# Kernel tuning notes

Measured on AMD Instinct MI355X. Metric: run time of the kernel, lower is better.

The kernel has to match this reference:

```python
import jax, jax.numpy as jnp
import numpy as np

N = 10000      # nodes
E = 160000     # edges (before self-loops)
IN = 128       # input channels
H1, C1 = 8, 128   # layer-1 heads / per-head channels
OUT = 64       # output channels
NEG_SLOPE = 0.2   # PyG GATConv leaky_relu slope


def _glorot(key, shape):
    fan = shape[0] + shape[-1]
    return jax.random.normal(key, shape, jnp.float32) * np.float32(np.sqrt(2.0 / fan))


def setup_inputs() -> dict:
    key = jax.random.key(0)
    ks = jax.random.split(key, 10)
    x = jax.random.normal(ks[0], (N, IN), jnp.float32)
    edge_index = jax.random.randint(ks[1], (2, E), 0, N, dtype=jnp.int64)
    return {
        "x": x,
        "edge_index": edge_index,
        "W1": _glorot(ks[2], (IN, H1 * C1)),
        "a_src1": _glorot(ks[3], (H1, C1)),
        "a_dst1": _glorot(ks[4], (H1, C1)),
        "b1": jnp.zeros((H1 * C1,), jnp.float32),
        "W2": _glorot(ks[5], (H1 * C1, OUT)),
        "a_src2": _glorot(ks[6], (1, OUT)),
        "a_dst2": _glorot(ks[7], (1, OUT)),
        "b2": jnp.zeros((OUT,), jnp.float32),
    }


def gat_conv(x, src, dst, W, a_src, a_dst, bias, heads, ch, concat):
    n = x.shape[0]
    h = (x @ W).reshape(n, heads, ch)                 # [N,H,C]
    alpha_s = jnp.sum(h * a_src, axis=-1)             # [N,H]
    alpha_d = jnp.sum(h * a_dst, axis=-1)             # [N,H]
    e = jax.nn.leaky_relu(alpha_s[src] + alpha_d[dst], NEG_SLOPE)  # [E',H]
    # segment softmax over incoming edges of each dst node
    m = jax.ops.segment_max(e, dst, num_segments=n)
    e = jnp.exp(e - m[dst])
    s = jax.ops.segment_sum(e, dst, num_segments=n)
    alpha = e / (s[dst] + 1e-16)                      # [E',H]
    msg = h[src] * alpha[:, :, None]                  # [E',H,C]
    out = jax.ops.segment_sum(msg, dst, num_segments=n)  # [N,H,C]
    out = out.reshape(n, heads * ch) if concat else jnp.mean(out, axis=1)
    return out + bias


def reference(x, edge_index, W1, a_src1, a_dst1, b1, W2, a_src2, a_dst2, b2):
    n = x.shape[0]
    loops = jnp.arange(n, dtype=edge_index.dtype)     # PyG add_self_loops=True
    src = jnp.concatenate([edge_index[0], loops])
    dst = jnp.concatenate([edge_index[1], loops])
    h = jax.nn.elu(gat_conv(x, src, dst, W1, a_src1, a_dst1, b1, H1, C1, True))
    # dropout is identity in eval mode
    return gat_conv(h, src, dst, W2, a_src2, a_dst2, b2, 1, OUT, False)
```

## Files before the change

### kernel.cpp

```cpp
#include <hip/hip_runtime.h>
#include <math.h>


#define NEG_SLOPE 0.2f

typedef short bf16x8 __attribute__((ext_vector_type(8)));
typedef float f32x4 __attribute__((ext_vector_type(4)));

__device__ __forceinline__ float leaky(float v) { return v >= 0.0f ? v : NEG_SLOPE * v; }

__device__ __forceinline__ unsigned short f2bf(float f) {
    unsigned u = __float_as_uint(f);
    u += 0x7FFFu + ((u >> 16) & 1u);
    return (unsigned short)(u >> 16);
}


__global__ __launch_bounds__(256) void prep_count(
    const float* __restrict__ W1, const float* __restrict__ a_src1,
    const float* __restrict__ a_dst1, const float* __restrict__ W2,
    const int* __restrict__ ei,
    float* __restrict__ As_t, float* __restrict__ Ad_t,
    unsigned short* __restrict__ W1bT, unsigned short* __restrict__ W2bT,
    int* __restrict__ counts, int E, int N) {
    int b = blockIdx.x;
    __shared__ unsigned short tile[32][33];
    if (b < 4) {
        int i = b * 256 + threadIdx.x;
        int k = i >> 3, h = i & 7;
        float ss = 0.f, sd = 0.f;
        for (int c = 0; c < 128; c += 4) {
            float4 w = *(const float4*)(W1 + (size_t)k * 1024 + h * 128 + c);
            float4 a = *(const float4*)(a_src1 + h * 128 + c);
            float4 d = *(const float4*)(a_dst1 + h * 128 + c);
            ss += w.x * a.x + w.y * a.y + w.z * a.z + w.w * a.w;
            sd += w.x * d.x + w.y * d.y + w.z * d.z + w.w * d.w;
        }
        As_t[h * 132 + k] = ss;
        Ad_t[h * 132 + k] = sd;
    } else if (b < 132) {
        int bb = b - 4;
        int kt = bb & 3, hct = bb >> 2;
        int j = threadIdx.x & 31;
        int i0 = threadIdx.x >> 5;
        for (int i = i0; i < 32; i += 8)
            tile[i][j] = f2bf(W1[(size_t)(kt * 32 + i) * 1024 + hct * 32 + j]);
        __syncthreads();
        for (int i = i0; i < 32; i += 8) {
            int hc = hct * 32 + i, k = kt * 32 + j;
            int h = hc >> 7, c = hc & 127;
            W1bT[h * 16384 + c * 128 + k] = tile[j][i];
        }
    } else if (b < 196) {
        int bb = b - 132;
        int kt = bb & 31, ctile = bb >> 5;
        int j = threadIdx.x & 31;
        int i0 = threadIdx.x >> 5;
        for (int i = i0; i < 32; i += 8)
            tile[i][j] = f2bf(W2[(size_t)(kt * 32 + i) * 64 + ctile * 32 + j]);
        __syncthreads();
        for (int i = i0; i < 32; i += 8)
            W2bT[(size_t)(ctile * 32 + i) * 1024 + kt * 32 + j] = tile[j][i];
    } else {
        int i = (b - 196) * 256 + threadIdx.x;
        int M = E + N;
        if (i >= M) return;
        int dst = (i < E) ? ei[E + i] : (i - E);
        atomicAdd(&counts[dst], 1);
    }
}


__global__ __launch_bounds__(1024) void alpha_scan(
    const float* __restrict__ x, const float* __restrict__ As_t, const float* __restrict__ Ad_t,
    float* __restrict__ as1, float* __restrict__ ad1,
    const int* __restrict__ counts, int* __restrict__ offsets,
    int* __restrict__ cursor, int N, int nb_alpha) {
    int t = threadIdx.x;
    if ((int)blockIdx.x < nb_alpha) {
        __shared__ float sAs[1056], sAd[1056];
        for (int i = t; i < 1056; i += 1024) {
            sAs[i] = As_t[i];
            sAd[i] = Ad_t[i];
        }
        __syncthreads();
        int node = blockIdx.x * 128 + (t >> 3);
        int h = t & 7;
        if (node >= N) return;
        const float* sa = sAs + h * 132;
        const float* sd = sAd + h * 132;
        float accs = 0.f, accd = 0.f;
        for (int k = 0; k < 128; k += 4) {
            float4 xv = *(const float4*)(x + (size_t)node * 128 + k);
            float4 av = *(const float4*)(sa + k);
            float4 dv = *(const float4*)(sd + k);
            accs += xv.x * av.x + xv.y * av.y + xv.z * av.z + xv.w * av.w;
            accd += xv.x * dv.x + xv.y * dv.y + xv.z * dv.z + xv.w * dv.w;
        }
        as1[node * 8 + h] = accs;
        ad1[node * 8 + h] = accd;
    } else {
        __shared__ int wsum[16];
        int per = (N + 1023) / 1024;
        int base = t * per;
        int s = 0;
        for (int j = 0; j < per; j++) {
            int idx = base + j;
            if (idx < N) s += counts[idx];
        }
        int lane = t & 63, wid = t >> 6;
        int inc = s;
#pragma unroll
        for (int off = 1; off <= 32; off <<= 1) {
            int v = __shfl_up(inc, off);
            if (lane >= off) inc += v;
        }
        if (lane == 63) wsum[wid] = inc;
        __syncthreads();
        if (t < 16) {
            int v = wsum[t];
            int iv = v;
#pragma unroll
            for (int off = 1; off <= 8; off <<= 1) {
                int u = __shfl_up(iv, off);
                if (t >= off) iv += u;
            }
            wsum[t] = iv - v;
        }
        __syncthreads();
        int run = wsum[wid] + inc - s;
        for (int j = 0; j < per; j++) {
            int idx = base + j;
            if (idx < N) {
                offsets[idx] = run;
                cursor[idx] = run;
                run += counts[idx];
            }
        }
        if (t == 1023) offsets[N] = run;
    }
}


__global__ __launch_bounds__(256) void fill_w1(
    const int* __restrict__ ei, int* __restrict__ cursor,
    const float* __restrict__ as1, const float* __restrict__ ad1,
    int* __restrict__ srcs, float* __restrict__ wbuf, int E, int N) {
    int i = blockIdx.x * blockDim.x + threadIdx.x;
    int M = E + N;
    if (i >= M) return;
    int src, dst;
    if (i < E) { src = ei[i]; dst = ei[E + i]; }
    else       { src = dst = i - E; }
    int pos = atomicAdd(&cursor[dst], 1);
    srcs[pos] = src;
    float4 a0 = *(const float4*)(as1 + (size_t)src * 8);
    float4 a1 = *(const float4*)(as1 + (size_t)src * 8 + 4);
    float4 b0 = *(const float4*)(ad1 + (size_t)dst * 8);
    float4 b1 = *(const float4*)(ad1 + (size_t)dst * 8 + 4);
    float4 w0, w1;
    w0.x = __expf(leaky(a0.x + b0.x));
    w0.y = __expf(leaky(a0.y + b0.y));
    w0.z = __expf(leaky(a0.z + b0.z));
    w0.w = __expf(leaky(a0.w + b0.w));
    w1.x = __expf(leaky(a1.x + b1.x));
    w1.y = __expf(leaky(a1.y + b1.y));
    w1.z = __expf(leaky(a1.z + b1.z));
    w1.w = __expf(leaky(a1.w + b1.w));
    *(float4*)(wbuf + (size_t)pos * 8)     = w0;
    *(float4*)(wbuf + (size_t)pos * 8 + 4) = w1;
}


__global__ __launch_bounds__(256) void l1_gather(
    const float* __restrict__ x, const float* __restrict__ wbuf,
    const int* __restrict__ offsets, const int* __restrict__ srcs,
    unsigned short* __restrict__ y_b, int N) {
    int n = blockIdx.x * 4 + (threadIdx.x >> 6);
    if (n >= N) return;
    int lane = threadIdx.x & 63;
    int beg = offsets[n];
    int deg = offsets[n + 1] - beg;
    float2 acc[8];
#pragma unroll
    for (int h = 0; h < 8; h++) acc[h] = make_float2(0.f, 0.f);
    float4 ws0 = make_float4(0.f, 0.f, 0.f, 0.f);
    float4 ws1 = make_float4(0.f, 0.f, 0.f, 0.f);
    const float* xb = x + lane * 2;
#define L1G_BODY(I)                                                              \
    {                                                                            \
        int s_ = srcs[beg + (I)];                                                \
        float4 w0_ = *(const float4*)(wbuf + (size_t)(beg + (I)) * 8);           \
        float4 w1_ = *(const float4*)(wbuf + (size_t)(beg + (I)) * 8 + 4);       \
        float2 xv_ = *(const float2*)(xb + (size_t)s_ * 128);                    \
        ws0.x += w0_.x; ws0.y += w0_.y; ws0.z += w0_.z; ws0.w += w0_.w;          \
        ws1.x += w1_.x; ws1.y += w1_.y; ws1.z += w1_.z; ws1.w += w1_.w;          \
        acc[0].x = fmaf(w0_.x, xv_.x, acc[0].x); acc[0].y = fmaf(w0_.x, xv_.y, acc[0].y); \
        acc[1].x = fmaf(w0_.y, xv_.x, acc[1].x); acc[1].y = fmaf(w0_.y, xv_.y, acc[1].y); \
        acc[2].x = fmaf(w0_.z, xv_.x, acc[2].x); acc[2].y = fmaf(w0_.z, xv_.y, acc[2].y); \
        acc[3].x = fmaf(w0_.w, xv_.x, acc[3].x); acc[3].y = fmaf(w0_.w, xv_.y, acc[3].y); \
        acc[4].x = fmaf(w1_.x, xv_.x, acc[4].x); acc[4].y = fmaf(w1_.x, xv_.y, acc[4].y); \
        acc[5].x = fmaf(w1_.y, xv_.x, acc[5].x); acc[5].y = fmaf(w1_.y, xv_.y, acc[5].y); \
        acc[6].x = fmaf(w1_.z, xv_.x, acc[6].x); acc[6].y = fmaf(w1_.z, xv_.y, acc[6].y); \
        acc[7].x = fmaf(w1_.w, xv_.x, acc[7].x); acc[7].y = fmaf(w1_.w, xv_.y, acc[7].y); \
    }
    int i = 0;
    for (; i + 4 <= deg; i += 4) {
        L1G_BODY(i) L1G_BODY(i + 1) L1G_BODY(i + 2) L1G_BODY(i + 3)
    }
    for (; i < deg; i++) { L1G_BODY(i) }
#undef L1G_BODY
    float inv[8] = {1.f / (ws0.x + 1e-16f), 1.f / (ws0.y + 1e-16f),
                    1.f / (ws0.z + 1e-16f), 1.f / (ws0.w + 1e-16f),
                    1.f / (ws1.x + 1e-16f), 1.f / (ws1.y + 1e-16f),
                    1.f / (ws1.z + 1e-16f), 1.f / (ws1.w + 1e-16f)};
    unsigned short* dst = y_b + (size_t)n * 1024 + lane * 2;
#pragma unroll
    for (int h = 0; h < 8; h++) {
        unsigned lo = f2bf(acc[h].x * inv[h]);
        unsigned hi = f2bf(acc[h].y * inv[h]);
        *(unsigned*)(dst + h * 128) = lo | (hi << 16);
    }
}


__global__ __launch_bounds__(256) void l12_gemm(
    const unsigned short* __restrict__ y_b, const unsigned short* __restrict__ W1bT,
    const float* __restrict__ b1, const unsigned short* __restrict__ W2bT,
    const float* __restrict__ a_src2, const float* __restrict__ a_dst2,
    float* __restrict__ h2, float* __restrict__ as2, float* __restrict__ ad2, int N) {
    int nb = blockIdx.x * 16;
    int w = threadIdx.x >> 6;
    int lane = threadIdx.x & 63;
    int n16 = lane & 15, quad = lane >> 4;
    __shared__ unsigned short hb[16 * 1032];
    __shared__ float sA[4][16], sD[4][16];
    int node_a = nb + n16;
    const unsigned short* yrow = y_b + (size_t)(node_a < N ? node_a : 0) * 1024;
#pragma unroll
    for (int cti = 0; cti < 16; cti++) {
        int ct = w * 16 + cti;
        int h = ct >> 3;
        int cc = (ct & 7) * 16;
        const unsigned short* Wh = W1bT + h * 16384 + (size_t)(cc + n16) * 128 + quad * 8;
        const unsigned short* ya = yrow + h * 128 + quad * 8;
        f32x4 acc = (f32x4){0.f, 0.f, 0.f, 0.f};
#pragma unroll
        for (int ks = 0; ks < 4; ks++) {
            bf16x8 a = *(const bf16x8*)(ya + ks * 32);
            bf16x8 b = *(const bf16x8*)(Wh + ks * 32);
            acc = __builtin_amdgcn_mfma_f32_16x16x32_bf16(a, b, acc, 0, 0, 0);
        }
        int c = h * 128 + cc + n16;
        float bias = b1[c];
#pragma unroll
        for (int r = 0; r < 4; r++) {
            float v = acc[r] + bias;
            v = v > 0.f ? v : expm1f(v);
            hb[(quad * 4 + r) * 1032 + c] = f2bf(v);
        }
    }
    __syncthreads();
    const unsigned short* arow = hb + n16 * 1032 + quad * 8;
    const unsigned short* brow = W2bT + (size_t)(w * 16 + n16) * 1024 + quad * 8;
    f32x4 acc = (f32x4){0.f, 0.f, 0.f, 0.f};
#pragma unroll 8
    for (int ks = 0; ks < 32; ks++) {
        bf16x8 a = *(const bf16x8*)(arow + ks * 32);
        bf16x8 b = *(const bf16x8*)(brow + ks * 32);
        acc = __builtin_amdgcn_mfma_f32_16x16x32_bf16(a, b, acc, 0, 0, 0);
    }
    int c2 = w * 16 + n16;
    float asc = a_src2[c2], adc = a_dst2[c2];
    float pav[4], pdv[4];
#pragma unroll
    for (int r = 0; r < 4; r++) {
        int node = nb + quad * 4 + r;
        if (node < N) h2[(size_t)node * 64 + c2] = acc[r];
        pav[r] = acc[r] * asc;
        pdv[r] = acc[r] * adc;
#pragma unroll
        for (int mm = 1; mm <= 8; mm <<= 1) {
            pav[r] += __shfl_xor(pav[r], mm);
            pdv[r] += __shfl_xor(pdv[r], mm);
        }
    }
    if (n16 == 0) {
#pragma unroll
        for (int r = 0; r < 4; r++) {
            sA[w][quad * 4 + r] = pav[r];
            sD[w][quad * 4 + r] = pdv[r];
        }
    }
    __syncthreads();
    if (threadIdx.x < 16) {
        int node = nb + threadIdx.x;
        if (node < N) {
            as2[node] = sA[0][threadIdx.x] + sA[1][threadIdx.x] + sA[2][threadIdx.x] + sA[3][threadIdx.x];
            ad2[node] = sD[0][threadIdx.x] + sD[1][threadIdx.x] + sD[2][threadIdx.x] + sD[3][threadIdx.x];
        }
    }
}


__global__ __launch_bounds__(256) void l2_gather(
    const float* __restrict__ h2, const float* __restrict__ as2,
    const float* __restrict__ ad2, const float* __restrict__ b2,
    const int* __restrict__ offsets, const int* __restrict__ srcs,
    float* __restrict__ out, int N) {
    int n = blockIdx.x * 4 + (threadIdx.x >> 6);
    if (n >= N) return;
    int lane = threadIdx.x & 63;
    int beg = offsets[n];
    int deg = offsets[n + 1] - beg;
    float adn = ad2[n];
    float acc = 0.f, wsum = 0.f;
    int i = 0;
    for (; i + 4 <= deg; i += 4) {
        int s0 = srcs[beg + i],     s1 = srcs[beg + i + 1];
        int s2 = srcs[beg + i + 2], s3 = srcs[beg + i + 3];
        float w0 = __expf(leaky(as2[s0] + adn));
        float w1 = __expf(leaky(as2[s1] + adn));
        float w2 = __expf(leaky(as2[s2] + adn));
        float w3 = __expf(leaky(as2[s3] + adn));
        float v0 = h2[(size_t)s0 * 64 + lane];
        float v1 = h2[(size_t)s1 * 64 + lane];
        float v2 = h2[(size_t)s2 * 64 + lane];
        float v3 = h2[(size_t)s3 * 64 + lane];
        wsum += w0 + w1 + w2 + w3;
        acc = fmaf(w0, v0, acc);
        acc = fmaf(w1, v1, acc);
        acc = fmaf(w2, v2, acc);
        acc = fmaf(w3, v3, acc);
    }
    for (; i < deg; i++) {
        int s = srcs[beg + i];
        float w = __expf(leaky(as2[s] + adn));
        wsum += w;
        acc = fmaf(w, h2[(size_t)s * 64 + lane], acc);
    }
    out[(size_t)n * 64 + lane] = acc / (wsum + 1e-16f) + b2[lane];
}


static inline size_t align_up(size_t v, size_t a) { return (v + a - 1) / a * a; }

extern "C" void kernel_launch(void* const* d_in, const int* in_sizes, int n_in,
                              void* d_out, int out_size, void* d_ws, size_t ws_size,
                              hipStream_t stream) {
    const float* x      = (const float*)d_in[0];
    const int*   ei     = (const int*)d_in[1];
    const float* W1     = (const float*)d_in[2];
    const float* a_src1 = (const float*)d_in[3];
    const float* a_dst1 = (const float*)d_in[4];
    const float* b1     = (const float*)d_in[5];
    const float* W2     = (const float*)d_in[6];
    const float* a_src2 = (const float*)d_in[7];
    const float* a_dst2 = (const float*)d_in[8];
    const float* b2     = (const float*)d_in[9];
    float* out = (float*)d_out;

    int N = in_sizes[0] / 128;
    int E = in_sizes[1] / 2;
    int M = E + N;

    char* p = (char*)d_ws;
    size_t off = 0;
    auto carve = [&](size_t bytes) {
        void* r = p + off;
        off = align_up(off + bytes, 256);
        return r;
    };
    int*            counts  = (int*)carve((size_t)N * 4);
    int*            offsets = (int*)carve((size_t)(N + 1) * 4);
    int*            cursor  = (int*)carve((size_t)N * 4);
    int*            srcs    = (int*)carve((size_t)M * 4);
    float*          As_t    = (float*)carve(1056 * 4);
    float*          Ad_t    = (float*)carve(1056 * 4);
    float*          as1     = (float*)carve((size_t)N * 8 * 4);
    float*          ad1     = (float*)carve((size_t)N * 8 * 4);
    float*          as2     = (float*)carve((size_t)N * 4);
    float*          ad2     = (float*)carve((size_t)N * 4);
    float*          h2      = (float*)carve((size_t)N * 64 * 4);
    float*          wbuf    = (float*)carve((size_t)M * 8 * 4);
    unsigned short* W1bT    = (unsigned short*)carve((size_t)8 * 128 * 128 * 2);
    unsigned short* W2bT    = (unsigned short*)carve((size_t)64 * 1024 * 2);
    unsigned short* y_b     = (unsigned short*)carve((size_t)N * 1024 * 2);
    (void)ws_size;

    int nb_count = (M + 255) / 256;
    int nb_alpha = (N + 127) / 128;

    hipMemsetAsync(counts, 0, (size_t)N * 4, stream);
    prep_count<<<196 + nb_count, 256, 0, stream>>>(W1, a_src1, a_dst1, W2, ei,
                                                   As_t, Ad_t, W1bT, W2bT, counts, E, N);
    alpha_scan<<<nb_alpha + 1, 1024, 0, stream>>>(x, As_t, Ad_t, as1, ad1,
                                                  counts, offsets, cursor, N, nb_alpha);
    fill_w1<<<nb_count, 256, 0, stream>>>(ei, cursor, as1, ad1, srcs, wbuf, E, N);
    l1_gather<<<(N + 3) / 4, 256, 0, stream>>>(x, wbuf, offsets, srcs, y_b, N);
    l12_gemm<<<(N + 15) / 16, 256, 0, stream>>>(y_b, W1bT, b1, W2bT, a_src2, a_dst2,
                                                h2, as2, ad2, N);
    l2_gather<<<(N + 3) / 4, 256, 0, stream>>>(h2, as2, ad2, b2, offsets, srcs, out, N);
}
```

Before: 192.7 us.

## Fuse layer-1 gather into GEMM kernel via LDS and shuffle-broadcast edge sources

Merges the layer-1 neighbor aggregation into the layer-1/2 GEMM kernel. Each block aggregates its 16 nodes into shared memory instead of writing bf16 rows to a global buffer, which removes one launch and the global write and read of y_b. In both gathers, each lane loads one edge source index and the index is broadcast with wave shuffles instead of repeated scalar loads. The layer-2 gather also computes one attention weight per lane and reduces the sum with xor shuffles. The cost is that the fused kernel roughly doubles its LDS use (about 66KB per block), which can lower occupancy. Each wave also processes its four nodes one after another, so gather latency is less hidden.

Measured after the change: 204.5 us. 6.1% more time.

```diff
diff --git a/kernel.cpp b/kernel.cpp
--- a/kernel.cpp
+++ b/kernel.cpp
@@ -172,27 +172,36 @@
 }
 
 
-__global__ __launch_bounds__(256) void l1_gather(
+__global__ __launch_bounds__(256) void l1g12(
     const float* __restrict__ x, const float* __restrict__ wbuf,
     const int* __restrict__ offsets, const int* __restrict__ srcs,
-    unsigned short* __restrict__ y_b, int N) {
-    int n = blockIdx.x * 4 + (threadIdx.x >> 6);
-    if (n >= N) return;
+    const unsigned short* __restrict__ W1bT, const float* __restrict__ b1,
+    const unsigned short* __restrict__ W2bT,
+    const float* __restrict__ a_src2, const float* __restrict__ a_dst2,
+    float* __restrict__ h2, float* __restrict__ as2, float* __restrict__ ad2, int N) {
+    int nb = blockIdx.x * 16;
+    int w = threadIdx.x >> 6;
     int lane = threadIdx.x & 63;
-    int beg = offsets[n];
-    int deg = offsets[n + 1] - beg;
-    float2 acc[8];
-#pragma unroll
-    for (int h = 0; h < 8; h++) acc[h] = make_float2(0.f, 0.f);
-    float4 ws0 = make_float4(0.f, 0.f, 0.f, 0.f);
-    float4 ws1 = make_float4(0.f, 0.f, 0.f, 0.f);
+    int n16 = lane & 15, quad = lane >> 4;
+    __shared__ unsigned short yls[16 * 1032];
+    __shared__ unsigned short hb[16 * 1032];
+    __shared__ float sA[4][16], sD[4][16];
+
     const float* xb = x + lane * 2;
-#define L1G_BODY(I)                                                              \
+    for (int j = 0; j < 4; j++) {
+        int n = nb + w * 4 + j;
+        float2 acc[8];
+#pragma unroll
+        for (int h = 0; h < 8; h++) acc[h] = make_float2(0.f, 0.f);
+        float4 ws0 = make_float4(0.f, 0.f, 0.f, 0.f);
+        float4 ws1 = make_float4(0.f, 0.f, 0.f, 0.f);
+        int beg = 0, deg = 0;
+        if (n < N) { beg = offsets[n]; deg = offsets[n + 1] - beg; }
+#define L1_FMA(EIDX, SRC)                                                        \
     {                                                                            \
-        int s_ = srcs[beg + (I)];                                                \
-        float4 w0_ = *(const float4*)(wbuf + (size_t)(beg + (I)) * 8);           \
-        float4 w1_ = *(const float4*)(wbuf + (size_t)(beg + (I)) * 8 + 4);       \
-        float2 xv_ = *(const float2*)(xb + (size_t)s_ * 128);                    \
+        float4 w0_ = *(const float4*)(wbuf + (size_t)(EIDX) * 8);                \
+        float4 w1_ = *(const float4*)(wbuf + (size_t)(EIDX) * 8 + 4);            \
+        float2 xv_ = *(const float2*)(xb + (size_t)(SRC) * 128);                 \
         ws0.x += w0_.x; ws0.y += w0_.y; ws0.z += w0_.z; ws0.w += w0_.w;          \
         ws1.x += w1_.x; ws1.y += w1_.y; ws1.z += w1_.z; ws1.w += w1_.w;          \
         acc[0].x = fmaf(w0_.x, xv_.x, acc[0].x); acc[0].y = fmaf(w0_.x, xv_.y, acc[0].y); \
@@ -204,39 +213,45 @@
         acc[6].x = fmaf(w1_.z, xv_.x, acc[6].x); acc[6].y = fmaf(w1_.z, xv_.y, acc[6].y); \
         acc[7].x = fmaf(w1_.w, xv_.x, acc[7].x); acc[7].y = fmaf(w1_.w, xv_.y, acc[7].y); \
     }
-    int i = 0;
-    for (; i + 4 <= deg; i += 4) {
-        L1G_BODY(i) L1G_BODY(i + 1) L1G_BODY(i + 2) L1G_BODY(i + 3)
-    }
-    for (; i < deg; i++) { L1G_BODY(i) }
-#undef L1G_BODY
-    float inv[8] = {1.f / (ws0.x + 1e-16f), 1.f / (ws0.y + 1e-16f),
-                    1.f / (ws0.z + 1e-16f), 1.f / (ws0.w + 1e-16f),
-                    1.f / (ws1.x + 1e-16f), 1.f / (ws1.y + 1e-16f),
-                    1.f / (ws1.z + 1e-16f), 1.f / (ws1.w + 1e-16f)};
-    unsigned short* dst = y_b + (size_t)n * 1024 + lane * 2;
-#pragma unroll
-    for (int h = 0; h < 8; h++) {
-        unsigned lo = f2bf(acc[h].x * inv[h]);
-        unsigned hi = f2bf(acc[h].y * inv[h]);
-        *(unsigned*)(dst + h * 128) = lo | (hi << 16);
-    }
-}
-
-
-__global__ __launch_bounds__(256) void l12_gemm(
-    const unsigned short* __restrict__ y_b, const unsigned short* __restrict__ W1bT,
-    const float* __restrict__ b1, const unsigned short* __restrict__ W2bT,
-    const float* __restrict__ a_src2, const float* __restrict__ a_dst2,
-    float* __restrict__ h2, float* __restrict__ as2, float* __restrict__ ad2, int N) {
-    int nb = blockIdx.x * 16;
-    int w = threadIdx.x >> 6;
-    int lane = threadIdx.x & 63;
-    int n16 = lane & 15, quad = lane >> 4;
-    __shared__ unsigned short hb[16 * 1032];
-    __shared__ float sA[4][16], sD[4][16];
-    int node_a = nb + n16;
-    const unsigned short* yrow = y_b + (size_t)(node_a < N ? node_a : 0) * 1024;
+        if (deg <= 64) {
+            int sv = srcs[beg + (lane < deg ? lane : 0)];
+            int i = 0;
+            for (; i + 4 <= deg; i += 4) {
+                int s0 = __shfl(sv, i);
+                int s1 = __shfl(sv, i + 1);
+                int s2 = __shfl(sv, i + 2);
+                int s3 = __shfl(sv, i + 3);
+                L1_FMA(beg + i, s0)
+                L1_FMA(beg + i + 1, s1)
+                L1_FMA(beg + i + 2, s2)
+                L1_FMA(beg + i + 3, s3)
+            }
+            for (; i < deg; i++) {
+                int s = __shfl(sv, i);
+                L1_FMA(beg + i, s)
+            }
+        } else {
+            for (int i = 0; i < deg; i++) {
+                int s = srcs[beg + i];
+                L1_FMA(beg + i, s)
+            }
+        }
+#undef L1_FMA
+        float inv[8] = {1.f / (ws0.x + 1e-16f), 1.f / (ws0.y + 1e-16f),
+                        1.f / (ws0.z + 1e-16f), 1.f / (ws0.w + 1e-16f),
+                        1.f / (ws1.x + 1e-16f), 1.f / (ws1.y + 1e-16f),
+                        1.f / (ws1.z + 1e-16f), 1.f / (ws1.w + 1e-16f)};
+        unsigned short* drow = &yls[(w * 4 + j) * 1032 + lane * 2];
+#pragma unroll
+        for (int h = 0; h < 8; h++) {
+            unsigned lo = f2bf(acc[h].x * inv[h]);
+            unsigned hi = f2bf(acc[h].y * inv[h]);
+            *(unsigned*)(drow + h * 128) = lo | (hi << 16);
+        }
+    }
+    __syncthreads();
+
+    const unsigned short* yrow = &yls[n16 * 1032];
 #pragma unroll
     for (int cti = 0; cti < 16; cti++) {
         int ct = w * 16 + cti;
@@ -261,6 +276,7 @@
         }
     }
     __syncthreads();
+
     const unsigned short* arow = hb + n16 * 1032 + quad * 8;
     const unsigned short* brow = W2bT + (size_t)(w * 16 + n16) * 1024 + quad * 8;
     f32x4 acc = (f32x4){0.f, 0.f, 0.f, 0.f};
@@ -314,30 +330,42 @@
     int beg = offsets[n];
     int deg = offsets[n + 1] - beg;
     float adn = ad2[n];
-    float acc = 0.f, wsum = 0.f;
-    int i = 0;
-    for (; i + 4 <= deg; i += 4) {
-        int s0 = srcs[beg + i],     s1 = srcs[beg + i + 1];
-        int s2 = srcs[beg + i + 2], s3 = srcs[beg + i + 3];
-        float w0 = __expf(leaky(as2[s0] + adn));
-        float w1 = __expf(leaky(as2[s1] + adn));
-        float w2 = __expf(leaky(as2[s2] + adn));
-        float w3 = __expf(leaky(as2[s3] + adn));
-        float v0 = h2[(size_t)s0 * 64 + lane];
-        float v1 = h2[(size_t)s1 * 64 + lane];
-        float v2 = h2[(size_t)s2 * 64 + lane];
-        float v3 = h2[(size_t)s3 * 64 + lane];
-        wsum += w0 + w1 + w2 + w3;
-        acc = fmaf(w0, v0, acc);
-        acc = fmaf(w1, v1, acc);
-        acc = fmaf(w2, v2, acc);
-        acc = fmaf(w3, v3, acc);
-    }
-    for (; i < deg; i++) {
-        int s = srcs[beg + i];
-        float w = __expf(leaky(as2[s] + adn));
-        wsum += w;
-        acc = fmaf(w, h2[(size_t)s * 64 + lane], acc);
+    float acc = 0.f, wsum;
+    if (deg <= 64) {
+        int sv = srcs[beg + (lane < deg ? lane : 0)];
+        float wv = (lane < deg) ? __expf(leaky(as2[sv] + adn)) : 0.f;
+        int i = 0;
+        for (; i + 4 <= deg; i += 4) {
+            int s0 = __shfl(sv, i),     s1 = __shfl(sv, i + 1);
+            int s2 = __shfl(sv, i + 2), s3 = __shfl(sv, i + 3);
+            float w0 = __shfl(wv, i),     w1 = __shfl(wv, i + 1);
+            float w2 = __shfl(wv, i + 2), w3 = __shfl(wv, i + 3);
+            float v0 = h2[(size_t)s0 * 64 + lane];
+            float v1 = h2[(size_t)s1 * 64 + lane];
+            float v2 = h2[(size_t)s2 * 64 + lane];
+            float v3 = h2[(size_t)s3 * 64 + lane];
+            acc = fmaf(w0, v0, acc);
+            acc = fmaf(w1, v1, acc);
+            acc = fmaf(w2, v2, acc);
+            acc = fmaf(w3, v3, acc);
+        }
+        for (; i < deg; i++) {
+            int s = __shfl(sv, i);
+            float ww = __shfl(wv, i);
+            acc = fmaf(ww, h2[(size_t)s * 64 + lane], acc);
+        }
+        float t = wv;
+#pragma unroll
+        for (int mm = 1; mm <= 32; mm <<= 1) t += __shfl_xor(t, mm);
+        wsum = t;
+    } else {
+        wsum = 0.f;
+        for (int i = 0; i < deg; i++) {
+            int s = srcs[beg + i];
+            float ww = __expf(leaky(as2[s] + adn));
+            wsum += ww;
+            acc = fmaf(ww, h2[(size_t)s * 64 + lane], acc);
+        }
     }
     out[(size_t)n * 64 + lane] = acc / (wsum + 1e-16f) + b2[lane];
 }
@@ -385,7 +413,6 @@
     float*          wbuf    = (float*)carve((size_t)M * 8 * 4);
     unsigned short* W1bT    = (unsigned short*)carve((size_t)8 * 128 * 128 * 2);
     unsigned short* W2bT    = (unsigned short*)carve((size_t)64 * 1024 * 2);
-    unsigned short* y_b     = (unsigned short*)carve((size_t)N * 1024 * 2);
     (void)ws_size;
 
     int nb_count = (M + 255) / 256;
@@ -397,8 +424,7 @@
     alpha_scan<<<nb_alpha + 1, 1024, 0, stream>>>(x, As_t, Ad_t, as1, ad1,
                                                   counts, offsets, cursor, N, nb_alpha);
     fill_w1<<<nb_count, 256, 0, stream>>>(ei, cursor, as1, ad1, srcs, wbuf, E, N);
-    l1_gather<<<(N + 3) / 4, 256, 0, stream>>>(x, wbuf, offsets, srcs, y_b, N);
-    l12_gemm<<<(N + 15) / 16, 256, 0, stream>>>(y_b, W1bT, b1, W2bT, a_src2, a_dst2,
-                                                h2, as2, ad2, N);
+    l1g12<<<(N + 15) / 16, 256, 0, stream>>>(x, wbuf, offsets, srcs, W1bT, b1, W2bT,
+                                             a_src2, a_dst2, h2, as2, ad2, N);
     l2_gather<<<(N + 3) / 4, 256, 0, stream>>>(h2, as2, ad2, b2, offsets, srcs, out, N);
 }
```
